# Kernel optimization log

Measured on AMD Instinct MI355X. Metric: run time of the kernel, lower is better.

The kernel has to match this reference:

```python
import jax, jax.numpy as jnp
import numpy as np

MIN_SIZE = 16.0
PH, PW, SCALE = 7, 7, 0.0625


def _context_anchor(rois, hh, hw):
    """rois: [N,5] (batch_idx,x1,y1,x2,y2). Returns [N*8,5] context boxes, col0 = 0 label."""
    N = rois.shape[0]
    x1, y1, x2, y2 = rois[:, 1], rois[:, 2], rois[:, 3], rois[:, 4]
    w, h = x2 - x1, y2 - y1
    k = jnp.arange(3, dtype=rois.dtype)
    sx = x1[:, None] + w[:, None] * (k - 0.5)  # x1 - w + w*k + w/2
    sy = y1[:, None] + h[:, None] * (k - 0.5)
    # np.meshgrid(shift_x, shift_y).ravel() is y-major
    cx = jnp.broadcast_to(sx[:, None, :], (N, 3, 3)).reshape(N, 9)
    cy = jnp.broadcast_to(sy[:, :, None], (N, 3, 3)).reshape(N, 9)
    boxes = jnp.stack([cx - w[:, None] / 4, cy - h[:, None] / 4,
                       cx + w[:, None] / 4, cy + h[:, None] / 4], -1)  # [N,9,4]
    bw = boxes[..., 2] - boxes[..., 0] + 1
    bh = boxes[..., 3] - boxes[..., 1] + 1
    invalid = ((boxes[..., 0] < 0) | (boxes[..., 1] < 0) |
               (boxes[..., 2] >= hw) | (boxes[..., 3] >= hh) |
               (bw < MIN_SIZE) | (bh < MIN_SIZE))
    boxes = jnp.where(invalid[..., None], rois[:, None, 1:5], boxes)
    boxes = boxes[:, jnp.array([0, 1, 2, 3, 5, 6, 7, 8]), :]  # drop center cell
    gt = boxes.reshape(N * 8, 4)  # K = 8N
    # IoU(all roi boxes, gt) with +1 pixel convention (bbox_overlaps_batch)
    A = rois[:, 1:5]
    aw, ah = A[:, 2] - A[:, 0] + 1, A[:, 3] - A[:, 1] + 1
    gw, gh = gt[:, 2] - gt[:, 0] + 1, gt[:, 3] - gt[:, 1] + 1
    iw = jnp.maximum(jnp.minimum(A[:, None, 2], gt[None, :, 2]) - jnp.maximum(A[:, None, 0], gt[None, :, 0]) + 1, 0)
    ih = jnp.maximum(jnp.minimum(A[:, None, 3], gt[None, :, 3]) - jnp.maximum(A[:, None, 1], gt[None, :, 1]) + 1, 0)
    inter = iw * ih
    ov = inter / ((aw * ah)[:, None] + (gw * gh)[None, :] - inter)  # [N,K]
    ov = jnp.where(((gw == 1) & (gh == 1))[None, :], 0.0, ov)
    ov = jnp.where(((aw == 1) & (ah == 1))[:, None], -1.0, ov)
    gt_max = ov.max(0)          # best overlap per gt box
    best = ov.argmax(0)         # index of best-matching roi (torch's `_`)
    labels = gt_max >= 0.3
    w_cell, h_cell = gt[:, 2] - gt[:, 0], gt[:, 3] - gt[:, 1]
    rw = jnp.where(labels, rois[best, 3] - rois[best, 1], 0.0)
    rh = jnp.where(labels, rois[best, 4] - rois[best, 2], 0.0)
    labels = (labels & ~(jnp.maximum(rw, rh) >= jnp.maximum(w_cell, h_cell))
                     & ~(jnp.minimum(rw, rh) < jnp.minimum(w_cell, h_cell) / 3))
    gt = jnp.where(labels[:, None], rois[best][:, 1:5], gt)
    # original zeroes labels at the end -> label column is all zeros
    return jnp.concatenate([jnp.zeros((N * 8, 1), rois.dtype), gt], -1)


def _roi_pool(features, boxes, ph, pw, scale):
    """Classic Caffe max RoIPool. Assumes batch_size==1 (all batch indices 0)."""
    _, C, H, W = features.shape
    f = features[0]  # [C,H,W]
    sw = jnp.round(boxes[:, 1] * scale)
    sh = jnp.round(boxes[:, 2] * scale)
    ew = jnp.round(boxes[:, 3] * scale)
    eh = jnp.round(boxes[:, 4] * scale)
    bsh = jnp.maximum(eh - sh + 1, 1.0) / ph
    bsw = jnp.maximum(ew - sw + 1, 1.0) / pw
    ii = jnp.arange(ph, dtype=f.dtype)
    jj = jnp.arange(pw, dtype=f.dtype)
    hs = jnp.clip(jnp.floor(ii[None, :] * bsh[:, None]) + sh[:, None], 0, H)   # [R,ph]
    he = jnp.clip(jnp.ceil((ii[None, :] + 1) * bsh[:, None]) + sh[:, None], 0, H)
    ws = jnp.clip(jnp.floor(jj[None, :] * bsw[:, None]) + sw[:, None], 0, W)   # [R,pw]
    we = jnp.clip(jnp.ceil((jj[None, :] + 1) * bsw[:, None]) + sw[:, None], 0, W)
    hidx = jnp.arange(H, dtype=f.dtype)
    widx = jnp.arange(W, dtype=f.dtype)
    mask_h = (hidx >= hs[..., None]) & (hidx < he[..., None])  # [R,ph,H]
    mask_w = (widx >= ws[..., None]) & (widx < we[..., None])  # [R,pw,W]
    NEG = jnp.asarray(-1e30, f.dtype)
    # separable masked max: reduce W per pw-bin, then H per ph-bin
    colmax = jnp.stack([jnp.where(mask_w[:, j, None, None, :], f[None], NEG).max(-1)
                        for j in range(pw)], axis=1)           # [R,pw,C,H]
    out = jnp.stack([jnp.where(mask_h[:, i, None, None, :], colmax, NEG).max(-1)
                     for i in range(ph)], axis=1)              # [R,ph,pw,C]
    valid = mask_h.any(-1)[:, :, None] & mask_w.any(-1)[:, None, :]
    out = jnp.where(valid[..., None], out, 0.0)                # empty bins -> 0
    return jnp.transpose(out, (0, 3, 1, 2))                    # [R,C,ph,pw]


def reference(features, rois, hh, hw):
    N = rois.shape[0]
    gt = _context_anchor(rois, hh, hw).reshape(N, 8, 5)
    cat_rois = jnp.concatenate([rois[:, None, :], gt], 1).reshape(-1, 5)  # [9N,5]
    pool = _roi_pool(features, cat_rois, PH, PW, SCALE)                   # [9N,C,7,7]
    pool_feat = pool.reshape(N, -1, PW, PH)                               # [N,9C,7,7]
    return pool_feat, cat_rois


def setup_inputs() -> dict:
    key = jax.random.key(0)
    k1, k2, k3, k4, k5 = jax.random.split(key, 5)
    N, C, Hf, Wf, IMG = 32, 256, 40, 40, 640
    x1 = jax.random.uniform(k1, (N,), minval=0.0, maxval=IMG - 220.0)
    y1 = jax.random.uniform(k2, (N,), minval=0.0, maxval=IMG - 220.0)
    bw = jax.random.uniform(k3, (N,), minval=80.0, maxval=200.0)
    bh = jax.random.uniform(k4, (N,), minval=80.0, maxval=200.0)
    rois = jnp.stack([jnp.zeros((N,)), x1, y1, x1 + bw, y1 + bh], -1).astype(jnp.float32)
    features = jax.random.normal(k5, (1, C, Hf, Wf), dtype=jnp.float32)
    return {"features": features, "rois": rois, "hh": 640, "hw": 640}
```

## Files before the change

### kernel.cpp

```cpp
#include <hip/hip_runtime.h>
#include <math.h>

#define N_ROIS   32
#define N_CAT    (N_ROIS * 9)
#define C_FEAT   256
#define H_FEAT   40
#define W_FEAT   40
#define P_FEAT   (H_FEAT * W_FEAT)
#define PH       7
#define PW       7
#define SCALE    0.0625f
#define MIN_SIZE 16.0f
#define CELLS    (PH * PW)
#define POOL_PER_BOX (C_FEAT * CELLS)
#define OUT_POOL_ELEMS ((size_t)N_CAT * POOL_PER_BOX)

#define N_TRANS_BLOCKS (P_FEAT / 32 * (C_FEAT / 32))
#define WIN 14

__global__ void prep_kernel(const float* __restrict__ f,
                            const float* __restrict__ rois,
                            const int* __restrict__ hh_p,
                            const int* __restrict__ hw_p,
                            float* __restrict__ ft,
                            float* __restrict__ cat_out,
                            int use_transpose) {
    __shared__ float tile[32][33];
    __shared__ float R[N_ROIS * 5];
    const int bid = blockIdx.x;
    const int tid = threadIdx.x;

    if (bid < N_TRANS_BLOCKS) {
        if (!use_transpose) return;
        const int pt = (bid % (P_FEAT / 32)) * 32;
        const int ct = (bid / (P_FEAT / 32)) * 32;
        const int lx = tid & 31;
        const int ly = tid >> 5;
        #pragma unroll
        for (int i = 0; i < 32; i += 8)
            tile[ly + i][lx] = f[(ct + ly + i) * P_FEAT + (pt + lx)];
        __syncthreads();
        #pragma unroll
        for (int i = 0; i < 32; i += 8)
            ft[(pt + ly + i) * C_FEAT + (ct + lx)] = tile[lx][ly + i];
        return;
    }

    if (tid < N_ROIS * 5) R[tid] = rois[tid];
    __syncthreads();

    const float hh = (float)(*hh_p);
    const float hw = (float)(*hw_p);

    const int g = tid;
    const int n = g >> 3;
    const int j = g & 7;
    const int m = (j < 4) ? j : j + 1;
    const int r  = m / 3;
    const int cc = m % 3;

    const float x1 = R[n * 5 + 1], y1 = R[n * 5 + 2];
    const float x2 = R[n * 5 + 3], y2 = R[n * 5 + 4];
    const float w = x2 - x1, h = y2 - y1;

    const float cx = x1 + w * ((float)cc - 0.5f);
    const float cy = y1 + h * ((float)r  - 0.5f);
    float bx1 = cx - w * 0.25f;
    float by1 = cy - h * 0.25f;
    float bx2 = cx + w * 0.25f;
    float by2 = cy + h * 0.25f;
    const float bw = bx2 - bx1 + 1.0f;
    const float bh = by2 - by1 + 1.0f;
    const bool invalid = (bx1 < 0.0f) || (by1 < 0.0f) ||
                         (bx2 >= hw) || (by2 >= hh) ||
                         (bw < MIN_SIZE) || (bh < MIN_SIZE);
    if (invalid) { bx1 = x1; by1 = y1; bx2 = x2; by2 = y2; }

    const float gw = bx2 - bx1 + 1.0f;
    const float gh = by2 - by1 + 1.0f;
    const float garea = gw * gh;
    const bool gdeg = (gw == 1.0f) && (gh == 1.0f);

    float best_ov = -INFINITY;
    int best = 0;
    for (int a = 0; a < N_ROIS; ++a) {
        const float ax1 = R[a * 5 + 1], ay1 = R[a * 5 + 2];
        const float ax2 = R[a * 5 + 3], ay2 = R[a * 5 + 4];
        const float aw = ax2 - ax1 + 1.0f, ah = ay2 - ay1 + 1.0f;
        float iw = fminf(ax2, bx2) - fmaxf(ax1, bx1) + 1.0f;
        float ih = fminf(ay2, by2) - fmaxf(ay1, by1) + 1.0f;
        iw = fmaxf(iw, 0.0f);
        ih = fmaxf(ih, 0.0f);
        const float inter = iw * ih;
        float ov = inter / (aw * ah + garea - inter);
        if (gdeg) ov = 0.0f;
        if (aw == 1.0f && ah == 1.0f) ov = -1.0f;
        if (ov > best_ov) { best_ov = ov; best = a; }
    }

    bool label = (best_ov >= 0.3f);
    const float w_cell = bx2 - bx1;
    const float h_cell = by2 - by1;
    const float rw = label ? (R[best * 5 + 3] - R[best * 5 + 1]) : 0.0f;
    const float rh = label ? (R[best * 5 + 4] - R[best * 5 + 2]) : 0.0f;
    label = label &&
            !(fmaxf(rw, rh) >= fmaxf(w_cell, h_cell)) &&
            !(fminf(rw, rh) < fminf(w_cell, h_cell) / 3.0f);
    if (label) {
        bx1 = R[best * 5 + 1]; by1 = R[best * 5 + 2];
        bx2 = R[best * 5 + 3]; by2 = R[best * 5 + 4];
    }

    float* row = cat_out + (size_t)(n * 9 + 1 + j) * 5;
    row[0] = 0.0f;
    row[1] = bx1; row[2] = by1; row[3] = bx2; row[4] = by2;
    if (j == 0) {
        float* rr = cat_out + (size_t)(n * 9) * 5;
        #pragma unroll
        for (int t = 0; t < 5; ++t) rr[t] = R[n * 5 + t];
    }
}

__global__ __launch_bounds__(256) void
roi_pool_kernel(const float* __restrict__ feat,
                const float* __restrict__ cat_rois,
                float* __restrict__ out) {
    const int i = blockIdx.x / N_CAT;
    const int b = blockIdx.x % N_CAT;
    const int c = threadIdx.x;

    const float* cr = cat_rois + (size_t)b * 5;
    const float x1 = cr[1], y1 = cr[2], x2 = cr[3], y2 = cr[4];
    const float sw = rintf(x1 * SCALE);
    const float sh = rintf(y1 * SCALE);
    const float ew = rintf(x2 * SCALE);
    const float eh = rintf(y2 * SCALE);
    const float bsh = fmaxf(eh - sh + 1.0f, 1.0f) * (1.0f / (float)PH);
    const float bsw = fmaxf(ew - sw + 1.0f, 1.0f) * (1.0f / (float)PW);

    const int hs = (int)fminf(fmaxf(floorf((float)i * bsh) + sh, 0.0f), (float)H_FEAT);
    const int he = (int)fminf(fmaxf(ceilf((float)(i + 1) * bsh) + sh, 0.0f), (float)H_FEAT);

    int ws[PW], we[PW];
    #pragma unroll
    for (int j = 0; j < PW; ++j) {
        ws[j] = (int)fminf(fmaxf(floorf((float)j * bsw) + sw, 0.0f), (float)W_FEAT);
        we[j] = (int)fminf(fmaxf(ceilf((float)(j + 1) * bsw) + sw, 0.0f), (float)W_FEAT);
    }

    const int xs = ws[0];
    const bool narrow = (bsw <= 2.0f);

    float mx[PW];
    #pragma unroll
    for (int j = 0; j < PW; ++j) mx[j] = -1e30f;

    if (narrow) {
        for (int y = hs; y < he; ++y) {
            const float* fr = feat + (size_t)(y * W_FEAT) * C_FEAT + c;
            float win[WIN];
            #pragma unroll
            for (int k = 0; k < WIN; ++k) {
                int x = xs + k;
                x = (x < W_FEAT - 1) ? x : (W_FEAT - 1);
                win[k] = fr[(size_t)x * C_FEAT];
            }
            #pragma unroll
            for (int j = 0; j < PW; ++j) {
                const int lo = ws[j], hi = we[j];
                const int kmax = (2 * j + 2 < WIN) ? (2 * j + 2) : WIN;
                #pragma unroll
                for (int k = 0; k < kmax; ++k) {
                    const int x = xs + k;
                    const bool in = (x >= lo) & (x < hi);
                    const float t = fmaxf(mx[j], win[k]);
                    mx[j] = in ? t : mx[j];
                }
            }
        }
    } else {
        for (int y = hs; y < he; ++y) {
            const float* fr = feat + (size_t)(y * W_FEAT) * C_FEAT + c;
            #pragma unroll
            for (int j = 0; j < PW; ++j)
                for (int x = ws[j]; x < we[j]; ++x)
                    mx[j] = fmaxf(mx[j], fr[(size_t)x * C_FEAT]);
        }
    }

    const bool rowv = (he > hs);
    float* ob = out + (size_t)b * POOL_PER_BOX + (size_t)c * CELLS + i * PW;
    #pragma unroll
    for (int j = 0; j < PW; ++j)
        ob[j] = (rowv && (we[j] > ws[j])) ? mx[j] : 0.0f;
}

__global__ __launch_bounds__(256) void
roi_pool_kernel_nchw(const float* __restrict__ feat,
                     const float* __restrict__ cat_rois,
                     float* __restrict__ out) {
    const int i = blockIdx.x / N_CAT;
    const int b = blockIdx.x % N_CAT;
    const int c = threadIdx.x;

    const float* cr = cat_rois + (size_t)b * 5;
    const float sw = rintf(cr[1] * SCALE);
    const float sh = rintf(cr[2] * SCALE);
    const float ew = rintf(cr[3] * SCALE);
    const float eh = rintf(cr[4] * SCALE);
    const float bsh = fmaxf(eh - sh + 1.0f, 1.0f) * (1.0f / (float)PH);
    const float bsw = fmaxf(ew - sw + 1.0f, 1.0f) * (1.0f / (float)PW);

    const int hs = (int)fminf(fmaxf(floorf((float)i * bsh) + sh, 0.0f), (float)H_FEAT);
    const int he = (int)fminf(fmaxf(ceilf((float)(i + 1) * bsh) + sh, 0.0f), (float)H_FEAT);
    int ws[PW], we[PW];
    #pragma unroll
    for (int j = 0; j < PW; ++j) {
        ws[j] = (int)fminf(fmaxf(floorf((float)j * bsw) + sw, 0.0f), (float)W_FEAT);
        we[j] = (int)fminf(fmaxf(ceilf((float)(j + 1) * bsw) + sw, 0.0f), (float)W_FEAT);
    }
    float mx[PW];
    #pragma unroll
    for (int j = 0; j < PW; ++j) mx[j] = -1e30f;
    for (int y = hs; y < he; ++y) {
        const float* fr = feat + (size_t)c * P_FEAT + y * W_FEAT;
        #pragma unroll
        for (int j = 0; j < PW; ++j)
            for (int x = ws[j]; x < we[j]; ++x)
                mx[j] = fmaxf(mx[j], fr[x]);
    }
    const bool rowv = (he > hs);
    float* ob = out + (size_t)b * POOL_PER_BOX + (size_t)c * CELLS + i * PW;
    #pragma unroll
    for (int j = 0; j < PW; ++j)
        ob[j] = (rowv && (we[j] > ws[j])) ? mx[j] : 0.0f;
}

extern "C" void kernel_launch(void* const* d_in, const int* in_sizes, int n_in,
                              void* d_out, int out_size, void* d_ws, size_t ws_size,
                              hipStream_t stream) {
    const float* features = (const float*)d_in[0];
    const float* rois     = (const float*)d_in[1];
    const int*   hh_p     = (const int*)d_in[2];
    const int*   hw_p     = (const int*)d_in[3];

    float* out      = (float*)d_out;
    float* cat_out  = out + OUT_POOL_ELEMS;
    float* ft       = (float*)d_ws;

    const size_t ft_bytes = (size_t)C_FEAT * P_FEAT * sizeof(float);
    const int use_transpose = (ws_size >= ft_bytes) ? 1 : 0;

    hipLaunchKernelGGL(prep_kernel, dim3(N_TRANS_BLOCKS + 1), dim3(256), 0, stream,
                       features, rois, hh_p, hw_p, ft, cat_out, use_transpose);

    if (use_transpose) {
        hipLaunchKernelGGL(roi_pool_kernel, dim3(PH * N_CAT), dim3(C_FEAT), 0, stream,
                           ft, cat_out, out);
    } else {
        hipLaunchKernelGGL(roi_pool_kernel_nchw, dim3(PH * N_CAT), dim3(C_FEAT), 0, stream,
                           features, cat_out, out);
    }
}
```

Baseline: 82.17 us.

## Stage ROI feature window in LDS and pool per channel-group with coalesced output

Replaces the per-row ROI pool kernel with one block per (box, 64-channel group) of 448 threads that handles all 7 pooled rows. For narrow boxes it stages a 14x14 pixel window of the transposed features into shared memory with float4 loads and computes maxima from LDS. Results are then staged in LDS so the output is written with coalesced float4 stores instead of strided scalar writes. The grid is also reordered to interleave boxes. This adds barriers and about 50KB of LDS per block, which lowers occupancy, and the window is only valid when both bin sizes are at most 2.

```diff
diff --git a/kernel.cpp b/kernel.cpp
--- a/kernel.cpp
+++ b/kernel.cpp
@@ -16,7 +16,19 @@
 #define OUT_POOL_ELEMS ((size_t)N_CAT * POOL_PER_BOX)
 
 #define N_TRANS_BLOCKS (P_FEAT / 32 * (C_FEAT / 32))
-#define WIN 14
+
+#define CH_G     64
+#define NCHG     4
+#define NBLK     (N_CAT * NCHG)
+#define TPB      448
+#define WROWS    14
+#define WCOLS    14
+#define PIX      (WROWS * WCOLS)
+#define SLOTS    (PIX + 2)
+#define WIN_FLTS (SLOTS * CH_G)
+#define OBUF_FLTS (CH_G * CELLS)
+#define QPP      (CH_G / 4)
+#define STAGE_N  (PIX * QPP)
 
 __global__ void prep_kernel(const float* __restrict__ f,
                             const float* __restrict__ rois,
@@ -121,78 +133,118 @@
     }
 }
 
-__global__ __launch_bounds__(256) void
-roi_pool_kernel(const float* __restrict__ feat,
-                const float* __restrict__ cat_rois,
-                float* __restrict__ out) {
-    const int i = blockIdx.x / N_CAT;
-    const int b = blockIdx.x % N_CAT;
-    const int c = threadIdx.x;
+__global__ __launch_bounds__(TPB) void
+pool_v8(const float* __restrict__ ft,
+        const float* __restrict__ cat_rois,
+        float* __restrict__ out) {
+    __shared__ __align__(16) float win[WIN_FLTS];
+
+    const int s   = (blockIdx.x & 7) * (NBLK / 8) + (blockIdx.x >> 3);
+    const int b   = s >> 2;
+    const int cg  = s & 3;
+    const int tid = threadIdx.x;
+    const int cl  = tid & 63;
+    const int i   = tid >> 6;
 
     const float* cr = cat_rois + (size_t)b * 5;
-    const float x1 = cr[1], y1 = cr[2], x2 = cr[3], y2 = cr[4];
-    const float sw = rintf(x1 * SCALE);
-    const float sh = rintf(y1 * SCALE);
-    const float ew = rintf(x2 * SCALE);
-    const float eh = rintf(y2 * SCALE);
+    const float bx1 = cr[1], by1 = cr[2], bx2 = cr[3], by2 = cr[4];
+    const float sw = rintf(bx1 * SCALE);
+    const float sh = rintf(by1 * SCALE);
+    const float ew = rintf(bx2 * SCALE);
+    const float eh = rintf(by2 * SCALE);
     const float bsh = fmaxf(eh - sh + 1.0f, 1.0f) * (1.0f / (float)PH);
     const float bsw = fmaxf(ew - sw + 1.0f, 1.0f) * (1.0f / (float)PW);
 
-    const int hs = (int)fminf(fmaxf(floorf((float)i * bsh) + sh, 0.0f), (float)H_FEAT);
-    const int he = (int)fminf(fmaxf(ceilf((float)(i + 1) * bsh) + sh, 0.0f), (float)H_FEAT);
+    const int hs = __builtin_amdgcn_readfirstlane(
+        (int)fminf(fmaxf(floorf((float)i * bsh) + sh, 0.0f), (float)H_FEAT));
+    const int he = __builtin_amdgcn_readfirstlane(
+        (int)fminf(fmaxf(ceilf((float)(i + 1) * bsh) + sh, 0.0f), (float)H_FEAT));
 
     int ws[PW], we[PW];
     #pragma unroll
     for (int j = 0; j < PW; ++j) {
-        ws[j] = (int)fminf(fmaxf(floorf((float)j * bsw) + sw, 0.0f), (float)W_FEAT);
-        we[j] = (int)fminf(fmaxf(ceilf((float)(j + 1) * bsw) + sw, 0.0f), (float)W_FEAT);
-    }
-
+        ws[j] = __builtin_amdgcn_readfirstlane(
+            (int)fminf(fmaxf(floorf((float)j * bsw) + sw, 0.0f), (float)W_FEAT));
+        we[j] = __builtin_amdgcn_readfirstlane(
+            (int)fminf(fmaxf(ceilf((float)(j + 1) * bsw) + sw, 0.0f), (float)W_FEAT));
+    }
     const int xs = ws[0];
-    const bool narrow = (bsw <= 2.0f);
-
-    float mx[PW];
-    #pragma unroll
-    for (int j = 0; j < PW; ++j) mx[j] = -1e30f;
+    const int ys = __builtin_amdgcn_readfirstlane(
+        (int)fminf(fmaxf(sh, 0.0f), (float)H_FEAT));
+
+    const bool narrow = (bsw <= 2.0f) && (bsh <= 2.0f);
+    const bool rowv = (he > hs);
 
     if (narrow) {
+        const float* fb = ft + cg * CH_G;
+        #pragma unroll
+        for (int t = 0; t < STAGE_N / TPB; ++t) {
+            const int e = tid + t * TPB;
+            const int q = e & (QPP - 1);
+            const int p = e >> 4;
+            const int py = p / WCOLS;
+            const int px = p - py * WCOLS;
+            const int gy = (ys + py < H_FEAT - 1) ? (ys + py) : (H_FEAT - 1);
+            const int gx = (xs + px < W_FEAT - 1) ? (xs + px) : (W_FEAT - 1);
+            const float4 v = *(const float4*)(fb + ((size_t)(gy * W_FEAT + gx)
+                                                    << 8) + (q << 2));
+            *(float4*)(win + p * CH_G + q * 4) = v;
+        }
+        __syncthreads();
+
+        float mx[PW];
+        #pragma unroll
+        for (int j = 0; j < PW; ++j) mx[j] = -1e30f;
+
+        int off[PW], nj[PW];
+        #pragma unroll
+        for (int j = 0; j < PW; ++j) {
+            off[j] = ws[j] - xs;
+            nj[j]  = we[j] - ws[j];
+        }
         for (int y = hs; y < he; ++y) {
-            const float* fr = feat + (size_t)(y * W_FEAT) * C_FEAT + c;
-            float win[WIN];
-            #pragma unroll
-            for (int k = 0; k < WIN; ++k) {
-                int x = xs + k;
-                x = (x < W_FEAT - 1) ? x : (W_FEAT - 1);
-                win[k] = fr[(size_t)x * C_FEAT];
-            }
+            const float* wr = win + (y - ys) * (WCOLS * CH_G) + cl;
             #pragma unroll
             for (int j = 0; j < PW; ++j) {
-                const int lo = ws[j], hi = we[j];
-                const int kmax = (2 * j + 2 < WIN) ? (2 * j + 2) : WIN;
-                #pragma unroll
-                for (int k = 0; k < kmax; ++k) {
-                    const int x = xs + k;
-                    const bool in = (x >= lo) & (x < hi);
-                    const float t = fmaxf(mx[j], win[k]);
-                    mx[j] = in ? t : mx[j];
-                }
+                const float* p0 = wr + off[j] * CH_G;
+                const float d0 = p0[0];
+                const float d1 = p0[CH_G];
+                const float d2 = p0[2 * CH_G];
+                if (nj[j] > 0) mx[j] = fmaxf(mx[j], d0);
+                if (nj[j] > 1) mx[j] = fmaxf(mx[j], d1);
+                if (nj[j] > 2) mx[j] = fmaxf(mx[j], d2);
             }
         }
+        __syncthreads();
+
+        float* orow = win + cl * CELLS + i * PW;
+        #pragma unroll
+        for (int j = 0; j < PW; ++j)
+            orow[j] = (rowv && (nj[j] > 0)) ? mx[j] : 0.0f;
+        __syncthreads();
+
+        const float4* src = (const float4*)win;
+        float4* dst = (float4*)(out + (size_t)b * POOL_PER_BOX
+                                    + (size_t)cg * OBUF_FLTS);
+        dst[tid] = src[tid];
+        const int e2 = tid + TPB;
+        if (e2 < OBUF_FLTS / 4) dst[e2] = src[e2];
     } else {
+        const int c = cg * CH_G + cl;
+        float mx[PW];
+        #pragma unroll
+        for (int j = 0; j < PW; ++j) mx[j] = -1e30f;
         for (int y = hs; y < he; ++y) {
-            const float* fr = feat + (size_t)(y * W_FEAT) * C_FEAT + c;
             #pragma unroll
             for (int j = 0; j < PW; ++j)
                 for (int x = ws[j]; x < we[j]; ++x)
-                    mx[j] = fmaxf(mx[j], fr[(size_t)x * C_FEAT]);
+                    mx[j] = fmaxf(mx[j], ft[(size_t)(y * W_FEAT + x) * C_FEAT + c]);
         }
-    }
-
-    const bool rowv = (he > hs);
-    float* ob = out + (size_t)b * POOL_PER_BOX + (size_t)c * CELLS + i * PW;
-    #pragma unroll
-    for (int j = 0; j < PW; ++j)
-        ob[j] = (rowv && (we[j] > ws[j])) ? mx[j] : 0.0f;
+        float* ob = out + (size_t)b * POOL_PER_BOX + (size_t)c * CELLS + i * PW;
+        #pragma unroll
+        for (int j = 0; j < PW; ++j)
+            ob[j] = (rowv && (we[j] > ws[j])) ? mx[j] : 0.0f;
+    }
 }
 
 __global__ __launch_bounds__(256) void
@@ -255,7 +307,7 @@
                        features, rois, hh_p, hw_p, ft, cat_out, use_transpose);
 
     if (use_transpose) {
-        hipLaunchKernelGGL(roi_pool_kernel, dim3(PH * N_CAT), dim3(C_FEAT), 0, stream,
+        hipLaunchKernelGGL(pool_v8, dim3(NBLK), dim3(TPB), 0, stream,
                            ft, cat_out, out);
     } else {
         hipLaunchKernelGGL(roi_pool_kernel_nchw, dim3(PH * N_CAT), dim3(C_FEAT), 0, stream,
```

Measured after the change: 79.59 us. 3.1% less time.
